# Kernel tuning notes

Hardware: AMD Instinct MI355X
Metric: run time of the kernel (lower is better)

The kernel has to match this reference:

```python
import jax, jax.numpy as jnp
import numpy as np

N_NODES = 100000
N_EDGES = 1200000
D = 64  # in = hid = out = 64


def _seg_sum(vals, idx, n):
    return jax.ops.segment_sum(vals, idx, num_segments=n)


def _graph_conv(x, src, dst, W, b, n_nodes):
    # dgl.nn.GraphConv with norm='both', bias=True:
    #   h = (D_out^-1/2 applied to src feats) -> sum over edges -> D_in^-1/2 -> +b
    # Weight applied first (math-equivalent linear, in==out dims here).
    e = src.shape[0]
    ones = jnp.ones((e,), x.dtype)
    deg_out = jnp.clip(_seg_sum(ones, src, n_nodes), 1.0)  # zero-deg clamp, as in DGL
    deg_in = jnp.clip(_seg_sum(ones, dst, n_nodes), 1.0)
    h = (x @ W) * jax.lax.rsqrt(deg_out)[:, None]          # [N, D]
    agg = _seg_sum(h[src], dst, n_nodes)                   # gather-scatter over edges
    return agg * jax.lax.rsqrt(deg_in)[:, None] + b


def _rgcn(x, edges, params, n_nodes):
    # HeteroGraphConv(aggregate='sum'): sum per-relation GraphConv outputs.
    (s0, d0), (s1, d1) = edges
    h = (_graph_conv(x, s0, d0, params['W1_0'], params['b1_0'], n_nodes)
         + _graph_conv(x, s1, d1, params['W1_1'], params['b1_1'], n_nodes))
    h = jax.nn.relu(h)
    h = (_graph_conv(h, s0, d0, params['W2_0'], params['b2_0'], n_nodes)
         + _graph_conv(h, s1, d1, params['W2_1'], params['b2_1'], n_nodes))
    return h


def setup_inputs() -> dict:
    key = jax.random.key(0)
    ks = jax.random.split(key, 16)
    inp = {
        'x': jax.random.normal(ks[0], (N_NODES, D), dtype=jnp.float32),
        'rel0_src': jax.random.randint(ks[1], (N_EDGES,), 0, N_NODES, dtype=jnp.int32),
        'rel0_dst': jax.random.randint(ks[2], (N_EDGES,), 0, N_NODES, dtype=jnp.int32),
        'rel1_src': jax.random.randint(ks[3], (N_EDGES,), 0, N_NODES, dtype=jnp.int32),
        'rel1_dst': jax.random.randint(ks[4], (N_EDGES,), 0, N_NODES, dtype=jnp.int32),
        'neg_src': jax.random.randint(ks[5], (N_EDGES,), 0, N_NODES, dtype=jnp.int32),
        'neg_dst': jax.random.randint(ks[6], (N_EDGES,), 0, N_NODES, dtype=jnp.int32),
    }
    scale = 1.0 / np.sqrt(D)
    for i, name in enumerate(['W1_0', 'W1_1', 'W2_0', 'W2_1']):
        inp[name] = jax.random.normal(ks[7 + i], (D, D), dtype=jnp.float32) * scale
    for name in ['b1_0', 'b1_1', 'b2_0', 'b2_1']:
        inp[name] = jnp.zeros((D,), dtype=jnp.float32)
    return inp


def reference(x, rel0_src, rel0_dst, rel1_src, rel1_dst, neg_src, neg_dst,
              W1_0, W1_1, W2_0, W2_1, b1_0, b1_1, b2_0, b2_1):
    params = {'W1_0': W1_0, 'b1_0': b1_0, 'W1_1': W1_1, 'b1_1': b1_1,
              'W2_0': W2_0, 'b2_0': b2_0, 'W2_1': W2_1, 'b2_1': b2_1}
    edges = ((rel0_src, rel0_dst), (rel1_src, rel1_dst))
    h = _rgcn(x, edges, params, N_NODES)  # [N, D]
    # HeteroDotProductPredictor: u_dot_v on etype edges -> [E, 1]
    pos_score = jnp.sum(h[rel0_src] * h[rel0_dst], axis=-1, keepdims=True)
    neg_score = jnp.sum(h[neg_src] * h[neg_dst], axis=-1, keepdims=True)
    return pos_score, neg_score
```

## Files before the change

kernel.cpp:

```cpp
#include <hip/hip_runtime.h>
#include <hip/hip_fp16.h>

#define N_NODES 100000
#define N_EDGES 1200000
#define TOTAL_E (2 * N_EDGES)
#define D 64

#define BSH 7
#define NBUCK 782
#define NCHUNK 320
#define CHUNK 7500
#define HIST_L (NBUCK * NCHUNK)
#define HIST2 (2 * HIST_L)
#define SCAN_BS 256
#define SCAN_NB2 ((HIST2 + SCAN_BS - 1) / SCAN_BS)
#define ENT_CAP 4608
#define L2M_GRID ((N_NODES + 127) / 128)
#define NKEY 2048

typedef __attribute__((ext_vector_type(8))) short bf16x8;
typedef __attribute__((ext_vector_type(4))) float f32x4;

__device__ __forceinline__ unsigned short f32_bf16_rne(float f) {
    unsigned u = __float_as_uint(f);
    unsigned r = u + 0x7FFF + ((u >> 16) & 1);
    return (unsigned short)(r >> 16);
}
__device__ __forceinline__ float bf16_f32(unsigned short h) {
    return __uint_as_float(((unsigned)h) << 16);
}

__global__ __launch_bounds__(512) void countA_kernel(const int* __restrict__ s0,
                                                     const int* __restrict__ d0,
                                                     const int* __restrict__ s1,
                                                     const int* __restrict__ d1,
                                                     int* __restrict__ hist) {
    __shared__ int hD[NBUCK];
    __shared__ int hS[NBUCK];
    int t = threadIdx.x;
    for (int i = t; i < NBUCK; i += 512) { hD[i] = 0; hS[i] = 0; }
    __syncthreads();
    int base = blockIdx.x * CHUNK;
    for (int i = t; i < CHUNK; i += 512) {
        int e = base + i;
        int rel = (e >= N_EDGES);
        int src = rel ? s1[e - N_EDGES] : s0[e];
        int dst = rel ? d1[e - N_EDGES] : d0[e];
        atomicAdd(&hD[dst >> BSH], 1);
        atomicAdd(&hS[src >> BSH], 1);
    }
    __syncthreads();
    for (int i = t; i < NBUCK; i += 512) {
        hist[i * NCHUNK + blockIdx.x] = hD[i];
        hist[HIST_L + i * NCHUNK + blockIdx.x] = hS[i];
    }
}

__global__ void scan1_kernel(const int* __restrict__ in, int* __restrict__ out,
                             int* __restrict__ bsum) {
    __shared__ int s[SCAN_BS];
    int t = threadIdx.x;
    int i = blockIdx.x * SCAN_BS + t;
    int v = (i < HIST2) ? in[i] : 0;
    s[t] = v;
    __syncthreads();
    for (int off = 1; off < SCAN_BS; off <<= 1) {
        int add = (t >= off) ? s[t - off] : 0;
        __syncthreads();
        s[t] += add;
        __syncthreads();
    }
    if (i < HIST2) out[i] = s[t] - v;
    if (t == SCAN_BS - 1) bsum[blockIdx.x] = s[t];
}

__global__ void scan2_kernel(int* __restrict__ bsum) {
    __shared__ int s[1024];
    int t = threadIdx.x;
    int v0 = (2 * t < SCAN_NB2) ? bsum[2 * t] : 0;
    int v1 = (2 * t + 1 < SCAN_NB2) ? bsum[2 * t + 1] : 0;
    int sum = v0 + v1;
    s[t] = sum;
    __syncthreads();
    for (int off = 1; off < 1024; off <<= 1) {
        int add = (t >= off) ? s[t - off] : 0;
        __syncthreads();
        s[t] += add;
        __syncthreads();
    }
    int ex = s[t] - sum;
    if (2 * t < SCAN_NB2) bsum[2 * t] = ex;
    if (2 * t + 1 < SCAN_NB2) bsum[2 * t + 1] = ex + v0;
}

__global__ void scan3_kernel(int* __restrict__ out, const int* __restrict__ bsum) {
    int i = blockIdx.x * SCAN_BS + threadIdx.x;
    if (i < HIST2) out[i] += bsum[blockIdx.x];
    if (i == 0) out[HIST2] = 2 * TOTAL_E;
}

__global__ __launch_bounds__(512) void scatterA_kernel(const int* __restrict__ s0,
                                                       const int* __restrict__ d0,
                                                       const int* __restrict__ s1,
                                                       const int* __restrict__ d1,
                                                       const int* __restrict__ OFS,
                                                       unsigned* __restrict__ binned,
                                                       unsigned char* __restrict__ binnedS) {
    __shared__ unsigned ent[CHUNK];
    __shared__ unsigned short kent[CHUNK];
    __shared__ int cnt[NBUCK], pfx[NBUCK], cur[NBUCK];
    __shared__ int tsum[512];
    int t = threadIdx.x, wg = blockIdx.x;
    int base = wg * CHUNK;

    for (int b = t; b < NBUCK; b += 512) cnt[b] = 0;
    __syncthreads();
    for (int i = t; i < CHUNK; i += 512) {
        int e = base + i;
        int rel = (e >= N_EDGES);
        int dst = rel ? d1[e - N_EDGES] : d0[e];
        atomicAdd(&cnt[dst >> BSH], 1);
    }
    __syncthreads();
    {
        int b2 = t * 2;
        int k0 = (b2 < NBUCK) ? cnt[b2] : 0;
        int k1 = (b2 + 1 < NBUCK) ? cnt[b2 + 1] : 0;
        int sum = k0 + k1;
        tsum[t] = sum;
        __syncthreads();
        for (int off = 1; off < 512; off <<= 1) {
            int add = (t >= off) ? tsum[t - off] : 0;
            __syncthreads();
            tsum[t] += add;
            __syncthreads();
        }
        int ex = tsum[t] - sum;
        if (b2 < NBUCK) pfx[b2] = ex;
        if (b2 + 1 < NBUCK) pfx[b2 + 1] = ex + k0;
    }
    __syncthreads();
    for (int b = t; b < NBUCK; b += 512) {
        cur[b] = pfx[b];
        cnt[b] = OFS[b * NCHUNK + wg];
    }
    __syncthreads();
    for (int i = t; i < CHUNK; i += 512) {
        int e = base + i;
        int rel = (e >= N_EDGES);
        int src = rel ? s1[e - N_EDGES] : s0[e];
        int dst = rel ? d1[e - N_EDGES] : d0[e];
        int kb = dst >> BSH;
        unsigned u = (unsigned)src | ((unsigned)(dst & 127) << 17) | ((unsigned)rel << 24);
        int r = atomicAdd(&cur[kb], 1);
        ent[r] = u;
        kent[r] = (unsigned short)kb;
    }
    __syncthreads();
    for (int j = t; j < CHUNK; j += 512) {
        int kb = (int)kent[j];
        binned[cnt[kb] + (j - pfx[kb])] = ent[j];
    }
    __syncthreads();
    for (int b = t; b < NBUCK; b += 512) cnt[b] = 0;
    __syncthreads();
    for (int i = t; i < CHUNK; i += 512)
        atomicAdd(&cnt[(int)(ent[i] & 0x1FFFFu) >> BSH], 1);
    __syncthreads();
    {
        int b2 = t * 2;
        int k0 = (b2 < NBUCK) ? cnt[b2] : 0;
        int k1 = (b2 + 1 < NBUCK) ? cnt[b2 + 1] : 0;
        int sum = k0 + k1;
        tsum[t] = sum;
        __syncthreads();
        for (int off = 1; off < 512; off <<= 1) {
            int add = (t >= off) ? tsum[t - off] : 0;
            __syncthreads();
            tsum[t] += add;
            __syncthreads();
        }
        int ex = tsum[t] - sum;
        if (b2 < NBUCK) pfx[b2] = ex;
        if (b2 + 1 < NBUCK) pfx[b2 + 1] = ex + k0;
    }
    __syncthreads();
    for (int b = t; b < NBUCK; b += 512) {
        cur[b] = pfx[b];
        cnt[b] = OFS[HIST_L + b * NCHUNK + wg] - TOTAL_E;
    }
    __syncthreads();
    for (int i = t; i < CHUNK; i += 512) {
        int kS = (int)(ent[i] & 0x1FFFFu) >> BSH;
        int r = atomicAdd(&cur[kS], 1);
        kent[r] = (unsigned short)i;
    }
    __syncthreads();
    for (int j = t; j < CHUNK; j += 512) {
        unsigned u = ent[(int)kent[j]];
        int kS = (int)(u & 0x1FFFFu) >> BSH;
        binnedS[cnt[kS] + (j - pfx[kS])] =
            (unsigned char)((u & 127) | (((u >> 24) & 1) << 7));
    }
}

__global__ __launch_bounds__(512) void sortB_kernel(unsigned* __restrict__ binned,
                                                    const int* __restrict__ OFS,
                                                    int* __restrict__ ip0,
                                                    int* __restrict__ ip1,
                                                    unsigned short* __restrict__ c0a,
                                                    unsigned short* __restrict__ c1a) {
    __shared__ unsigned ent[ENT_CAP];
    __shared__ int cnt[NKEY], pfx[NKEY], cur[NKEY];
    __shared__ int tsum[512];
    int t = threadIdx.x;
    int b = blockIdx.x;
    int start = OFS[b * NCHUNK];
    int end = OFS[(b + 1) * NCHUNK];
    int n = end - start;

    for (int i = t; i < NKEY; i += 512) cnt[i] = 0;
    __syncthreads();
    for (int i = t; i < n; i += 512) {
        unsigned u = binned[start + i];
        if (i < ENT_CAP) ent[i] = u;
        int key = ((int)((u >> 17) & 255) << 3) | (int)((u & 0x1FFFFu) >> 14);
        atomicAdd(&cnt[key], 1);
    }
    __syncthreads();
    int b4 = t * 4;
    int k0 = cnt[b4], k1 = cnt[b4 + 1], k2 = cnt[b4 + 2], k3 = cnt[b4 + 3];
    int s1 = k0 + k1, s2 = s1 + k2, s3 = s2 + k3;
    tsum[t] = s3;
    __syncthreads();
    for (int off = 1; off < 512; off <<= 1) {
        int add = (t >= off) ? tsum[t - off] : 0;
        __syncthreads();
        tsum[t] += add;
        __syncthreads();
    }
    int ex = tsum[t] - s3;
    pfx[b4] = ex;
    pfx[b4 + 1] = ex + k0;
    pfx[b4 + 2] = ex + s1;
    pfx[b4 + 3] = ex + s2;
    cur[b4] = ex;
    cur[b4 + 1] = ex + k0;
    cur[b4 + 2] = ex + s1;
    cur[b4 + 3] = ex + s2;
    __syncthreads();
    for (int i = t; i < n; i += 512) {
        if (i < ENT_CAP) {
            unsigned u = ent[i];
            int key = ((int)((u >> 17) & 255) << 3) | (int)((u & 0x1FFFFu) >> 14);
            int p = atomicAdd(&cur[key], 1);
            binned[start + p] = u & 0x1FFFF;
        }
    }
    if (t < 128) {
        int node = b * 128 + t;
        if (node < N_NODES) {
            int kr0 = t << 3;
            int kr1 = (1 << 10) | (t << 3);
            int p0 = pfx[kr0];
            int e0 = pfx[kr0 + 8];
            int p1 = pfx[kr1];
            int e1 = (t == 127) ? n : pfx[kr1 + 8];
            ip0[node] = start + p0;
            ip1[node] = start + p1;
            c0a[node] = (unsigned short)(e0 - p0);
            c1a[node] = (unsigned short)(e1 - p1);
        }
    }
}

__global__ __launch_bounds__(512) void countO_kernel(const unsigned char* __restrict__ binnedS,
                                                     const int* __restrict__ OFS,
                                                     int* __restrict__ cntO0,
                                                     int* __restrict__ cntO1) {
    __shared__ int cnt[256];
    int t = threadIdx.x;
    int b = blockIdx.x;
    int start = OFS[HIST_L + b * NCHUNK] - TOTAL_E;
    int end = OFS[HIST_L + (b + 1) * NCHUNK] - TOTAL_E;
    if (t < 256) cnt[t] = 0;
    __syncthreads();
    for (int i = start + t; i < end; i += 512)
        atomicAdd(&cnt[(int)binnedS[i]], 1);
    __syncthreads();
    if (t < 128) {
        int node = b * 128 + t;
        if (node < N_NODES) {
            cntO0[node] = cnt[t];
            cntO1[node] = cnt[t | 128];
        }
    }
}

__global__ void wprep_kernel(const float* __restrict__ W0,
                             const float* __restrict__ W1,
                             short* __restrict__ Wf) {
    int t = blockIdx.x * blockDim.x + threadIdx.x;
    if (t >= 2 * 4096) return;
    int rel = t >> 12;
    int e = t & 4095;
    int k = e >> 6, col = e & 63;
    float wv = (rel ? W1 : W0)[e];
    unsigned short hi = f32_bf16_rne(wv);
    unsigned short lo = f32_bf16_rne(wv - bf16_f32(hi));
    int kstep = k >> 5, g = (k >> 3) & 3, j = k & 7;
    int base = ((((rel * 2 + 0) * 2 + kstep) * 4 + g) * 64 + col) * 8 + j;
    int baseL = ((((rel * 2 + 1) * 2 + kstep) * 4 + g) * 64 + col) * 8 + j;
    Wf[base] = (short)hi;
    Wf[baseL] = (short)lo;
}

__global__ __launch_bounds__(256) void lin2m_kernel(const float* __restrict__ x,
                                                    const short* __restrict__ Wf,
                                                    const int* __restrict__ cntO0,
                                                    const int* __restrict__ cntO1,
                                                    __half* __restrict__ y0,
                                                    __half* __restrict__ y1) {
    int t = threadIdx.x;
    int w = t >> 6, lane = t & 63;
    int lr = lane & 15, g = lane >> 4;
    int rowbase = blockIdx.x * 128 + w * 32;

    bf16x8 ah[2][2], al[2][2];
#pragma unroll
    for (int m = 0; m < 2; ++m) {
        int row = rowbase + m * 16 + lr;
        bool ok = row < N_NODES;
        const float* xp = x + (size_t)row * 64 + g * 8;
#pragma unroll
        for (int s = 0; s < 2; ++s) {
            float fv[8];
            if (ok) {
                float4 f0 = ((const float4*)(xp + s * 32))[0];
                float4 f1 = ((const float4*)(xp + s * 32))[1];
                fv[0] = f0.x; fv[1] = f0.y; fv[2] = f0.z; fv[3] = f0.w;
                fv[4] = f1.x; fv[5] = f1.y; fv[6] = f1.z; fv[7] = f1.w;
            } else {
#pragma unroll
                for (int j = 0; j < 8; ++j) fv[j] = 0.f;
            }
#pragma unroll
            for (int j = 0; j < 8; ++j) {
                unsigned short hi = f32_bf16_rne(fv[j]);
                unsigned short lo = f32_bf16_rne(fv[j] - bf16_f32(hi));
                ah[m][s][j] = (short)hi;
                al[m][s][j] = (short)lo;
            }
        }
    }

    float rsc[2][2][4];
#pragma unroll
    for (int m = 0; m < 2; ++m)
#pragma unroll
        for (int reg = 0; reg < 4; ++reg) {
            int row = rowbase + m * 16 + g * 4 + reg;
            bool ok = row < N_NODES;
            rsc[0][m][reg] = ok ? rsqrtf((float)max(cntO0[row], 1)) : 1.f;
            rsc[1][m][reg] = ok ? rsqrtf((float)max(cntO1[row], 1)) : 1.f;
        }

#pragma unroll
    for (int rel = 0; rel < 2; ++rel) {
        __half* yo = rel ? y1 : y0;
        const short* wr = Wf + rel * 8192 + g * 512;
#pragma unroll
        for (int n = 0; n < 4; ++n) {
            const short* wb = wr + (n * 16 + lr) * 8;
            bf16x8 wh0 = *(const bf16x8*)(wb);
            bf16x8 wh1 = *(const bf16x8*)(wb + 2048);
            bf16x8 wl0 = *(const bf16x8*)(wb + 4096);
            bf16x8 wl1 = *(const bf16x8*)(wb + 6144);
#pragma unroll
            for (int m = 0; m < 2; ++m) {
                f32x4 acc = {0.f, 0.f, 0.f, 0.f};
                acc = __builtin_amdgcn_mfma_f32_16x16x32_bf16(al[m][0], wh0, acc, 0, 0, 0);
                acc = __builtin_amdgcn_mfma_f32_16x16x32_bf16(ah[m][0], wl0, acc, 0, 0, 0);
                acc = __builtin_amdgcn_mfma_f32_16x16x32_bf16(ah[m][0], wh0, acc, 0, 0, 0);
                acc = __builtin_amdgcn_mfma_f32_16x16x32_bf16(al[m][1], wh1, acc, 0, 0, 0);
                acc = __builtin_amdgcn_mfma_f32_16x16x32_bf16(ah[m][1], wl1, acc, 0, 0, 0);
                acc = __builtin_amdgcn_mfma_f32_16x16x32_bf16(ah[m][1], wh1, acc, 0, 0, 0);
#pragma unroll
                for (int reg = 0; reg < 4; ++reg) {
                    int row = rowbase + m * 16 + g * 4 + reg;
                    if (row < N_NODES)
                        yo[(size_t)row * 64 + n * 16 + lr] =
                            __float2half_rn(acc[reg] * rsc[rel][m][reg]);
                }
            }
        }
    }
}

template <int RELU, int OUTH>
__global__ __launch_bounds__(256) void aggC_kernel(const __half* __restrict__ L0,
                                                   const __half* __restrict__ L1,
                                                   const unsigned* __restrict__ es,
                                                   const int* __restrict__ ip0,
                                                   const int* __restrict__ ip1,
                                                   const unsigned short* __restrict__ c0a,
                                                   const unsigned short* __restrict__ c1a,
                                                   const float* __restrict__ bia0,
                                                   const float* __restrict__ bia1,
                                                   float* __restrict__ outf,
                                                   __half* __restrict__ outh) {
    int t = threadIdx.x;
    int g = t >> 3, l8 = t & 7;
    int node = blockIdx.x * 32 + g;
    if (node >= N_NODES) return;

    int st0 = ip0[node], c0 = c0a[node];
    int st1 = ip1[node], c1 = c1a[node];

    float a[8] = {0, 0, 0, 0, 0, 0, 0, 0};
    float a2[8] = {0, 0, 0, 0, 0, 0, 0, 0};
    float b[8] = {0, 0, 0, 0, 0, 0, 0, 0};
    float b2[8] = {0, 0, 0, 0, 0, 0, 0, 0};
    union HU { uint4 u; __half2 h[4]; };

    int k = 0;
    for (; k + 4 <= c0; k += 4) {
        int sA = (int)es[st0 + k];
        int sB = (int)es[st0 + k + 1];
        int sC = (int)es[st0 + k + 2];
        int sD = (int)es[st0 + k + 3];
        HU uA, uB, uC, uD;
        uA.u = ((const uint4*)(L0 + (size_t)sA * 64))[l8];
        uB.u = ((const uint4*)(L0 + (size_t)sB * 64))[l8];
        uC.u = ((const uint4*)(L0 + (size_t)sC * 64))[l8];
        uD.u = ((const uint4*)(L0 + (size_t)sD * 64))[l8];
#pragma unroll
        for (int q = 0; q < 4; ++q) {
            float2 fA = __half22float2(uA.h[q]);
            float2 fB = __half22float2(uB.h[q]);
            float2 fC = __half22float2(uC.h[q]);
            float2 fD = __half22float2(uD.h[q]);
            a[2 * q] += fA.x + fC.x;  a[2 * q + 1] += fA.y + fC.y;
            a2[2 * q] += fB.x + fD.x; a2[2 * q + 1] += fB.y + fD.y;
        }
    }
    for (; k < c0; ++k) {
        int s = (int)es[st0 + k];
        HU uu;
        uu.u = ((const uint4*)(L0 + (size_t)s * 64))[l8];
#pragma unroll
        for (int q = 0; q < 4; ++q) {
            float2 f = __half22float2(uu.h[q]);
            a[2 * q] += f.x;
            a[2 * q + 1] += f.y;
        }
    }
    k = 0;
    for (; k + 4 <= c1; k += 4) {
        int sA = (int)es[st1 + k];
        int sB = (int)es[st1 + k + 1];
        int sC = (int)es[st1 + k + 2];
        int sD = (int)es[st1 + k + 3];
        HU uA, uB, uC, uD;
        uA.u = ((const uint4*)(L1 + (size_t)sA * 64))[l8];
        uB.u = ((const uint4*)(L1 + (size_t)sB * 64))[l8];
        uC.u = ((const uint4*)(L1 + (size_t)sC * 64))[l8];
        uD.u = ((const uint4*)(L1 + (size_t)sD * 64))[l8];
#pragma unroll
        for (int q = 0; q < 4; ++q) {
            float2 fA = __half22float2(uA.h[q]);
            float2 fB = __half22float2(uB.h[q]);
            float2 fC = __half22float2(uC.h[q]);
            float2 fD = __half22float2(uD.h[q]);
            b[2 * q] += fA.x + fC.x;  b[2 * q + 1] += fA.y + fC.y;
            b2[2 * q] += fB.x + fD.x; b2[2 * q + 1] += fB.y + fD.y;
        }
    }
    for (; k < c1; ++k) {
        int s = (int)es[st1 + k];
        HU uu;
        uu.u = ((const uint4*)(L1 + (size_t)s * 64))[l8];
#pragma unroll
        for (int q = 0; q < 4; ++q) {
            float2 f = __half22float2(uu.h[q]);
            b[2 * q] += f.x;
            b[2 * q + 1] += f.y;
        }
    }

    float r0 = rsqrtf((float)max(c0, 1));
    float r1 = rsqrtf((float)max(c1, 1));
    float4 u0a = ((const float4*)bia0)[l8 * 2];
    float4 u0b = ((const float4*)bia0)[l8 * 2 + 1];
    float4 u1a = ((const float4*)bia1)[l8 * 2];
    float4 u1b = ((const float4*)bia1)[l8 * 2 + 1];
    float o[8];
#pragma unroll
    for (int q = 0; q < 8; ++q) o[q] = (a[q] + a2[q]) * r0 + (b[q] + b2[q]) * r1;
    o[0] += u0a.x + u1a.x; o[1] += u0a.y + u1a.y;
    o[2] += u0a.z + u1a.z; o[3] += u0a.w + u1a.w;
    o[4] += u0b.x + u1b.x; o[5] += u0b.y + u1b.y;
    o[6] += u0b.z + u1b.z; o[7] += u0b.w + u1b.w;
    if (RELU) {
#pragma unroll
        for (int q = 0; q < 8; ++q) o[q] = fmaxf(o[q], 0.f);
    }
    if (OUTH) {
        HU vv;
#pragma unroll
        for (int q = 0; q < 4; ++q)
            vv.h[q] = __floats2half2_rn(o[2 * q], o[2 * q + 1]);
        ((uint4*)(outh + (size_t)node * 64))[l8] = vv.u;
    } else {
        float4 f0 = {o[0], o[1], o[2], o[3]};
        float4 f1 = {o[4], o[5], o[6], o[7]};
        ((float4*)(outf + (size_t)node * 64))[l8 * 2] = f0;
        ((float4*)(outf + (size_t)node * 64))[l8 * 2 + 1] = f1;
    }
}

__global__ __launch_bounds__(256) void score_kernel(const __half* __restrict__ h2,
                                                    const int* __restrict__ ps,
                                                    const int* __restrict__ pd,
                                                    const int* __restrict__ ns,
                                                    const int* __restrict__ nd,
                                                    float* __restrict__ out) {
    int gid = blockIdx.x * blockDim.x + threadIdx.x;
    int pr = gid >> 3;
    int l8 = gid & 7;
    int e0 = pr * 2;
    if (e0 >= TOTAL_E) return;
    int e1 = e0 + 1;
    int sA, dA, sB, dB;
    if (e0 < N_EDGES) { sA = ps[e0]; dA = pd[e0]; sB = ps[e1]; dB = pd[e1]; }
    else {
        sA = ns[e0 - N_EDGES]; dA = nd[e0 - N_EDGES];
        sB = ns[e1 - N_EDGES]; dB = nd[e1 - N_EDGES];
    }
    union HU { uint4 u; __half2 h[4]; };
    HU ua0, ub0, ua1, ub1;
    ua0.u = ((const uint4*)(h2 + (size_t)sA * 64))[l8];
    ub0.u = ((const uint4*)(h2 + (size_t)dA * 64))[l8];
    ua1.u = ((const uint4*)(h2 + (size_t)sB * 64))[l8];
    ub1.u = ((const uint4*)(h2 + (size_t)dB * 64))[l8];
    float p0 = 0.f, p1 = 0.f;
#pragma unroll
    for (int q = 0; q < 4; ++q) {
        float2 fa0 = __half22float2(ua0.h[q]);
        float2 fb0 = __half22float2(ub0.h[q]);
        float2 fa1 = __half22float2(ua1.h[q]);
        float2 fb1 = __half22float2(ub1.h[q]);
        p0 += fa0.x * fb0.x + fa0.y * fb0.y;
        p1 += fa1.x * fb1.x + fa1.y * fb1.y;
    }
    p0 += __shfl_xor(p0, 1);
    p0 += __shfl_xor(p0, 2);
    p0 += __shfl_xor(p0, 4);
    p1 += __shfl_xor(p1, 1);
    p1 += __shfl_xor(p1, 2);
    p1 += __shfl_xor(p1, 4);
    if (l8 == 0) ((float2*)out)[pr] = make_float2(p0, p1);
}

extern "C" void kernel_launch(void* const* d_in, const int* in_sizes, int n_in,
                              void* d_out, int out_size, void* d_ws, size_t ws_size,
                              hipStream_t stream) {
    const float* x    = (const float*)d_in[0];
    const int* s0     = (const int*)d_in[1];
    const int* d0     = (const int*)d_in[2];
    const int* s1     = (const int*)d_in[3];
    const int* d1     = (const int*)d_in[4];
    const int* nsrc   = (const int*)d_in[5];
    const int* ndst   = (const int*)d_in[6];
    const float* W1_0 = (const float*)d_in[7];
    const float* W1_1 = (const float*)d_in[8];
    const float* W2_0 = (const float*)d_in[9];
    const float* W2_1 = (const float*)d_in[10];
    const float* b1_0 = (const float*)d_in[11];
    const float* b1_1 = (const float*)d_in[12];
    const float* b2_0 = (const float*)d_in[13];
    const float* b2_1 = (const float*)d_in[14];
    float* out = (float*)d_out;

    char* p = (char*)d_ws;
    int* cntO0 = (int*)p;      p += N_NODES * 4;
    int* cntO1 = (int*)p;      p += N_NODES * 4;
    int* hist  = (int*)p;      p += (size_t)HIST2 * 4;
    int* OFS   = (int*)p;      p += ((size_t)HIST2 + 8) * 4;
    int* bsum  = (int*)p;      p += 2048 * 4;
    unsigned* binned = (unsigned*)p;  p += (size_t)TOTAL_E * 4;
    int* ip0   = (int*)p;      p += N_NODES * 4;
    int* ip1   = (int*)p;      p += N_NODES * 4;
    unsigned short* c0a = (unsigned short*)p;  p += N_NODES * 2;
    unsigned short* c1a = (unsigned short*)p;  p += N_NODES * 2;
    unsigned char* binnedS = (unsigned char*)p;  p += (size_t)TOTAL_E;
    p = (char*)(((size_t)p + 255) & ~(size_t)255);
    short* WfA = (short*)p;    p += 16384 * 2;
    short* WfB = (short*)p;    p += 16384 * 2;
    p = (char*)(((size_t)p + 255) & ~(size_t)255);
    __half* bufL0h = (__half*)p;  p += (size_t)N_NODES * D * 2;
    __half* bufL1h = (__half*)p;  p += (size_t)N_NODES * D * 2;
    __half* h2h    = (__half*)p;  p += (size_t)N_NODES * D * 2;
    p = (char*)(((size_t)p + 255) & ~(size_t)255);
    float* bufH = (float*)p;   p += (size_t)N_NODES * D * 4;

    const int aggGrid  = (N_NODES + 31) / 32;
    const int scorGrid = (TOTAL_E / 2 * 8 + 255) / 256;

    wprep_kernel<<<32, 256, 0, stream>>>(W1_0, W1_1, WfA);
    wprep_kernel<<<32, 256, 0, stream>>>(W2_0, W2_1, WfB);

    countA_kernel<<<NCHUNK, 512, 0, stream>>>(s0, d0, s1, d1, hist);
    scan1_kernel<<<SCAN_NB2, SCAN_BS, 0, stream>>>(hist, OFS, bsum);
    scan2_kernel<<<1, 1024, 0, stream>>>(bsum);
    scan3_kernel<<<SCAN_NB2, SCAN_BS, 0, stream>>>(OFS, bsum);
    scatterA_kernel<<<NCHUNK, 512, 0, stream>>>(s0, d0, s1, d1, OFS, binned, binnedS);
    sortB_kernel<<<NBUCK, 512, 0, stream>>>(binned, OFS, ip0, ip1, c0a, c1a);
    countO_kernel<<<NBUCK, 512, 0, stream>>>(binnedS, OFS, cntO0, cntO1);

    lin2m_kernel<<<L2M_GRID, 256, 0, stream>>>(x, WfA, cntO0, cntO1, bufL0h, bufL1h);
    aggC_kernel<1, 0><<<aggGrid, 256, 0, stream>>>(bufL0h, bufL1h, binned, ip0, ip1,
                                                   c0a, c1a, b1_0, b1_1, bufH, nullptr);

    lin2m_kernel<<<L2M_GRID, 256, 0, stream>>>(bufH, WfB, cntO0, cntO1, bufL0h, bufL1h);
    aggC_kernel<0, 1><<<aggGrid, 256, 0, stream>>>(bufL0h, bufL1h, binned, ip0, ip1,
                                                   c0a, c1a, b2_0, b2_1, nullptr, h2h);

    score_kernel<<<scorGrid, 256, 0, stream>>>(h2h, s0, d0, nsrc, ndst, out);
}
```

Measured before the change: 273.3 us.

## Merge relation edge lists per node and gather in source-range phases

The edge sort now buckets each destination's incoming edges from both relations together, ordered by a coarse source-node range (13 phases), with the relation flag kept in bit 17. It records per-node phase counts. The aggregation kernel walks phases in lockstep across the block's 128 destination nodes, so concurrent gathers hit a narrower slice of the feature tables and should get better L2/cache locality. Per-edge degree scaling replaces the separate per-relation accumulators. The cost is a 16-entry count array per node, many more inner-loop iterations with small trip counts, and less unrolling (2 instead of 4), which may lower memory-level parallelism.

```diff
diff --git a/kernel.cpp b/kernel.cpp
--- a/kernel.cpp
+++ b/kernel.cpp
@@ -17,6 +17,7 @@
 #define ENT_CAP 4608
 #define L2M_GRID ((N_NODES + 127) / 128)
 #define NKEY 2048
+#define NPH 13
 
 typedef __attribute__((ext_vector_type(8))) short bf16x8;
 typedef __attribute__((ext_vector_type(4))) float f32x4;
@@ -206,12 +207,13 @@
 
 __global__ __launch_bounds__(512) void sortB_kernel(unsigned* __restrict__ binned,
                                                     const int* __restrict__ OFS,
-                                                    int* __restrict__ ip0,
-                                                    int* __restrict__ ip1,
+                                                    int* __restrict__ ip,
+                                                    unsigned short* __restrict__ cph,
                                                     unsigned short* __restrict__ c0a,
                                                     unsigned short* __restrict__ c1a) {
     __shared__ unsigned ent[ENT_CAP];
     __shared__ int cnt[NKEY], pfx[NKEY], cur[NKEY];
+    __shared__ int cnt2[256];
     __shared__ int tsum[512];
     int t = threadIdx.x;
     int b = blockIdx.x;
@@ -220,12 +222,15 @@
     int n = end - start;
 
     for (int i = t; i < NKEY; i += 512) cnt[i] = 0;
+    if (t < 256) cnt2[t] = 0;
     __syncthreads();
     for (int i = t; i < n; i += 512) {
         unsigned u = binned[start + i];
         if (i < ENT_CAP) ent[i] = u;
-        int key = ((int)((u >> 17) & 255) << 3) | (int)((u & 0x1FFFFu) >> 14);
-        atomicAdd(&cnt[key], 1);
+        int dl = (int)((u >> 17) & 127);
+        int ph = (int)((u & 0x1FFFFu) >> 13);
+        atomicAdd(&cnt[(dl << 4) | ph], 1);
+        atomicAdd(&cnt2[dl | (int)(((u >> 24) & 1) << 7)], 1);
     }
     __syncthreads();
     int b4 = t * 4;
@@ -252,24 +257,25 @@
     for (int i = t; i < n; i += 512) {
         if (i < ENT_CAP) {
             unsigned u = ent[i];
-            int key = ((int)((u >> 17) & 255) << 3) | (int)((u & 0x1FFFFu) >> 14);
-            int p = atomicAdd(&cur[key], 1);
-            binned[start + p] = u & 0x1FFFF;
+            int dl = (int)((u >> 17) & 127);
+            int ph = (int)((u & 0x1FFFFu) >> 13);
+            int p = atomicAdd(&cur[(dl << 4) | ph], 1);
+            binned[start + p] = (u & 0x1FFFFu) | (((u >> 24) & 1u) << 17);
         }
     }
     if (t < 128) {
         int node = b * 128 + t;
         if (node < N_NODES) {
-            int kr0 = t << 3;
-            int kr1 = (1 << 10) | (t << 3);
-            int p0 = pfx[kr0];
-            int e0 = pfx[kr0 + 8];
-            int p1 = pfx[kr1];
-            int e1 = (t == 127) ? n : pfx[kr1 + 8];
-            ip0[node] = start + p0;
-            ip1[node] = start + p1;
-            c0a[node] = (unsigned short)(e0 - p0);
-            c1a[node] = (unsigned short)(e1 - p1);
+            ip[node] = start + pfx[t << 4];
+            c0a[node] = (unsigned short)cnt2[t];
+            c1a[node] = (unsigned short)cnt2[t | 128];
+            unsigned short* cp = cph + (size_t)node * 16;
+#pragma unroll
+            for (int p2 = 0; p2 < 16; ++p2) {
+                int k = (t << 4) + p2;
+                int e2 = (k + 1 < NKEY) ? pfx[k + 1] : n;
+                cp[p2] = (unsigned short)((p2 < NPH) ? (e2 - pfx[k]) : 0);
+            }
         }
     }
 }
@@ -398,125 +404,114 @@
 }
 
 template <int RELU, int OUTH>
-__global__ __launch_bounds__(256) void aggC_kernel(const __half* __restrict__ L0,
+__global__ __launch_bounds__(512) void aggP_kernel(const __half* __restrict__ L0,
                                                    const __half* __restrict__ L1,
                                                    const unsigned* __restrict__ es,
-                                                   const int* __restrict__ ip0,
-                                                   const int* __restrict__ ip1,
+                                                   const int* __restrict__ ip,
+                                                   const unsigned short* __restrict__ cph,
                                                    const unsigned short* __restrict__ c0a,
                                                    const unsigned short* __restrict__ c1a,
                                                    const float* __restrict__ bia0,
                                                    const float* __restrict__ bia1,
                                                    float* __restrict__ outf,
                                                    __half* __restrict__ outh) {
-    int t = threadIdx.x;
+    int t = threadIdx.x, b = blockIdx.x;
     int g = t >> 3, l8 = t & 7;
-    int node = blockIdx.x * 32 + g;
-    if (node >= N_NODES) return;
-
-    int st0 = ip0[node], c0 = c0a[node];
-    int st1 = ip1[node], c1 = c1a[node];
-
-    float a[8] = {0, 0, 0, 0, 0, 0, 0, 0};
-    float a2[8] = {0, 0, 0, 0, 0, 0, 0, 0};
-    float b[8] = {0, 0, 0, 0, 0, 0, 0, 0};
-    float b2[8] = {0, 0, 0, 0, 0, 0, 0, 0};
+    int nA = b * 128 + g, nB = nA + 64;
+    bool vA = nA < N_NODES, vB = nB < N_NODES;
+    int curA = vA ? ip[nA] : 0;
+    int curB = vB ? ip[nB] : 0;
+    float rA0 = vA ? rsqrtf((float)max((int)c0a[nA], 1)) : 0.f;
+    float rA1 = vA ? rsqrtf((float)max((int)c1a[nA], 1)) : 0.f;
+    float rB0 = vB ? rsqrtf((float)max((int)c0a[nB], 1)) : 0.f;
+    float rB1 = vB ? rsqrtf((float)max((int)c1a[nB], 1)) : 0.f;
+    const unsigned short* cpA = cph + (size_t)nA * 16;
+    const unsigned short* cpB = cph + (size_t)nB * 16;
+
+    float oA[8] = {0, 0, 0, 0, 0, 0, 0, 0};
+    float oB[8] = {0, 0, 0, 0, 0, 0, 0, 0};
     union HU { uint4 u; __half2 h[4]; };
 
-    int k = 0;
-    for (; k + 4 <= c0; k += 4) {
-        int sA = (int)es[st0 + k];
-        int sB = (int)es[st0 + k + 1];
-        int sC = (int)es[st0 + k + 2];
-        int sD = (int)es[st0 + k + 3];
-        HU uA, uB, uC, uD;
-        uA.u = ((const uint4*)(L0 + (size_t)sA * 64))[l8];
-        uB.u = ((const uint4*)(L0 + (size_t)sB * 64))[l8];
-        uC.u = ((const uint4*)(L0 + (size_t)sC * 64))[l8];
-        uD.u = ((const uint4*)(L0 + (size_t)sD * 64))[l8];
-#pragma unroll
-        for (int q = 0; q < 4; ++q) {
-            float2 fA = __half22float2(uA.h[q]);
-            float2 fB = __half22float2(uB.h[q]);
-            float2 fC = __half22float2(uC.h[q]);
-            float2 fD = __half22float2(uD.h[q]);
-            a[2 * q] += fA.x + fC.x;  a[2 * q + 1] += fA.y + fC.y;
-            a2[2 * q] += fB.x + fD.x; a2[2 * q + 1] += fB.y + fD.y;
-        }
-    }
-    for (; k < c0; ++k) {
-        int s = (int)es[st0 + k];
-        HU uu;
-        uu.u = ((const uint4*)(L0 + (size_t)s * 64))[l8];
-#pragma unroll
-        for (int q = 0; q < 4; ++q) {
-            float2 f = __half22float2(uu.h[q]);
-            a[2 * q] += f.x;
-            a[2 * q + 1] += f.y;
-        }
-    }
-    k = 0;
-    for (; k + 4 <= c1; k += 4) {
-        int sA = (int)es[st1 + k];
-        int sB = (int)es[st1 + k + 1];
-        int sC = (int)es[st1 + k + 2];
-        int sD = (int)es[st1 + k + 3];
-        HU uA, uB, uC, uD;
-        uA.u = ((const uint4*)(L1 + (size_t)sA * 64))[l8];
-        uB.u = ((const uint4*)(L1 + (size_t)sB * 64))[l8];
-        uC.u = ((const uint4*)(L1 + (size_t)sC * 64))[l8];
-        uD.u = ((const uint4*)(L1 + (size_t)sD * 64))[l8];
-#pragma unroll
-        for (int q = 0; q < 4; ++q) {
-            float2 fA = __half22float2(uA.h[q]);
-            float2 fB = __half22float2(uB.h[q]);
-            float2 fC = __half22float2(uC.h[q]);
-            float2 fD = __half22float2(uD.h[q]);
-            b[2 * q] += fA.x + fC.x;  b[2 * q + 1] += fA.y + fC.y;
-            b2[2 * q] += fB.x + fD.x; b2[2 * q + 1] += fB.y + fD.y;
-        }
-    }
-    for (; k < c1; ++k) {
-        int s = (int)es[st1 + k];
-        HU uu;
-        uu.u = ((const uint4*)(L1 + (size_t)s * 64))[l8];
-#pragma unroll
-        for (int q = 0; q < 4; ++q) {
-            float2 f = __half22float2(uu.h[q]);
-            b[2 * q] += f.x;
-            b[2 * q + 1] += f.y;
-        }
-    }
-
-    float r0 = rsqrtf((float)max(c0, 1));
-    float r1 = rsqrtf((float)max(c1, 1));
+#define GATHER2(cur, c, o, r0_, r1_)                                          \
+    {                                                                         \
+        int k = 0;                                                            \
+        for (; k + 2 <= (c); k += 2) {                                        \
+            unsigned u1 = es[(cur) + k], u2 = es[(cur) + k + 1];              \
+            const __half* p1 = ((u1 >> 17) ? L1 : L0) + (size_t)(u1 & 0x1FFFFu) * 64; \
+            const __half* p2 = ((u2 >> 17) ? L1 : L0) + (size_t)(u2 & 0x1FFFFu) * 64; \
+            float sc1 = (u1 >> 17) ? (r1_) : (r0_);                           \
+            float sc2 = (u2 >> 17) ? (r1_) : (r0_);                           \
+            HU v1, v2;                                                        \
+            v1.u = ((const uint4*)p1)[l8];                                    \
+            v2.u = ((const uint4*)p2)[l8];                                    \
+            _Pragma("unroll")                                                 \
+            for (int q = 0; q < 4; ++q) {                                     \
+                float2 f1 = __half22float2(v1.h[q]);                          \
+                float2 f2 = __half22float2(v2.h[q]);                          \
+                (o)[2 * q] += f1.x * sc1 + f2.x * sc2;                        \
+                (o)[2 * q + 1] += f1.y * sc1 + f2.y * sc2;                    \
+            }                                                                 \
+        }                                                                     \
+        if (k < (c)) {                                                        \
+            unsigned u1 = es[(cur) + k];                                      \
+            const __half* p1 = ((u1 >> 17) ? L1 : L0) + (size_t)(u1 & 0x1FFFFu) * 64; \
+            float sc1 = (u1 >> 17) ? (r1_) : (r0_);                           \
+            HU v1;                                                            \
+            v1.u = ((const uint4*)p1)[l8];                                    \
+            _Pragma("unroll")                                                 \
+            for (int q = 0; q < 4; ++q) {                                     \
+                float2 f1 = __half22float2(v1.h[q]);                          \
+                (o)[2 * q] += f1.x * sc1;                                     \
+                (o)[2 * q + 1] += f1.y * sc1;                                 \
+            }                                                                 \
+        }                                                                     \
+    }
+
+    for (int p = 0; p < NPH; ++p) {
+        int cA = vA ? (int)cpA[p] : 0;
+        GATHER2(curA, cA, oA, rA0, rA1);
+        curA += cA;
+        int cB = vB ? (int)cpB[p] : 0;
+        GATHER2(curB, cB, oB, rB0, rB1);
+        curB += cB;
+    }
+#undef GATHER2
+
     float4 u0a = ((const float4*)bia0)[l8 * 2];
     float4 u0b = ((const float4*)bia0)[l8 * 2 + 1];
     float4 u1a = ((const float4*)bia1)[l8 * 2];
     float4 u1b = ((const float4*)bia1)[l8 * 2 + 1];
-    float o[8];
-#pragma unroll
-    for (int q = 0; q < 8; ++q) o[q] = (a[q] + a2[q]) * r0 + (b[q] + b2[q]) * r1;
-    o[0] += u0a.x + u1a.x; o[1] += u0a.y + u1a.y;
-    o[2] += u0a.z + u1a.z; o[3] += u0a.w + u1a.w;
-    o[4] += u0b.x + u1b.x; o[5] += u0b.y + u1b.y;
-    o[6] += u0b.z + u1b.z; o[7] += u0b.w + u1b.w;
-    if (RELU) {
-#pragma unroll
-        for (int q = 0; q < 8; ++q) o[q] = fmaxf(o[q], 0.f);
-    }
-    if (OUTH) {
-        HU vv;
-#pragma unroll
-        for (int q = 0; q < 4; ++q)
-            vv.h[q] = __floats2half2_rn(o[2 * q], o[2 * q + 1]);
-        ((uint4*)(outh + (size_t)node * 64))[l8] = vv.u;
-    } else {
-        float4 f0 = {o[0], o[1], o[2], o[3]};
-        float4 f1 = {o[4], o[5], o[6], o[7]};
-        ((float4*)(outf + (size_t)node * 64))[l8 * 2] = f0;
-        ((float4*)(outf + (size_t)node * 64))[l8 * 2 + 1] = f1;
-    }
+    float bs[8];
+    bs[0] = u0a.x + u1a.x; bs[1] = u0a.y + u1a.y;
+    bs[2] = u0a.z + u1a.z; bs[3] = u0a.w + u1a.w;
+    bs[4] = u0b.x + u1b.x; bs[5] = u0b.y + u1b.y;
+    bs[6] = u0b.z + u1b.z; bs[7] = u0b.w + u1b.w;
+
+#define STORE_NODE(valid, node, o)                                            \
+    if (valid) {                                                              \
+        float oo[8];                                                          \
+        _Pragma("unroll")                                                     \
+        for (int q = 0; q < 8; ++q) {                                         \
+            oo[q] = (o)[q] + bs[q];                                           \
+            if (RELU) oo[q] = fmaxf(oo[q], 0.f);                              \
+        }                                                                     \
+        if (OUTH) {                                                           \
+            HU vv;                                                            \
+            _Pragma("unroll")                                                 \
+            for (int q = 0; q < 4; ++q)                                       \
+                vv.h[q] = __floats2half2_rn(oo[2 * q], oo[2 * q + 1]);        \
+            ((uint4*)(outh + (size_t)(node) * 64))[l8] = vv.u;                \
+        } else {                                                              \
+            float4 f0 = {oo[0], oo[1], oo[2], oo[3]};                         \
+            float4 f1 = {oo[4], oo[5], oo[6], oo[7]};                         \
+            ((float4*)(outf + (size_t)(node) * 64))[l8 * 2] = f0;             \
+            ((float4*)(outf + (size_t)(node) * 64))[l8 * 2 + 1] = f1;         \
+        }                                                                     \
+    }
+
+    STORE_NODE(vA, nA, oA);
+    STORE_NODE(vB, nB, oB);
+#undef STORE_NODE
 }
 
 __global__ __launch_bounds__(256) void score_kernel(const __half* __restrict__ h2,
@@ -589,8 +584,8 @@
     int* OFS   = (int*)p;      p += ((size_t)HIST2 + 8) * 4;
     int* bsum  = (int*)p;      p += 2048 * 4;
     unsigned* binned = (unsigned*)p;  p += (size_t)TOTAL_E * 4;
-    int* ip0   = (int*)p;      p += N_NODES * 4;
-    int* ip1   = (int*)p;      p += N_NODES * 4;
+    int* ip    = (int*)p;      p += N_NODES * 4;
+    unsigned short* cph = (unsigned short*)p;  p += (size_t)(N_NODES) * 16 * 2;
     unsigned short* c0a = (unsigned short*)p;  p += N_NODES * 2;
     unsigned short* c1a = (unsigned short*)p;  p += N_NODES * 2;
     unsigned char* binnedS = (unsigned char*)p;  p += (size_t)TOTAL_E;
@@ -604,7 +599,6 @@
     p = (char*)(((size_t)p + 255) & ~(size_t)255);
     float* bufH = (float*)p;   p += (size_t)N_NODES * D * 4;
 
-    const int aggGrid  = (N_NODES + 31) / 32;
     const int scorGrid = (TOTAL_E / 2 * 8 + 255) / 256;
 
     wprep_kernel<<<32, 256, 0, stream>>>(W1_0, W1_1, WfA);
@@ -615,16 +609,16 @@
     scan2_kernel<<<1, 1024, 0, stream>>>(bsum);
     scan3_kernel<<<SCAN_NB2, SCAN_BS, 0, stream>>>(OFS, bsum);
     scatterA_kernel<<<NCHUNK, 512, 0, stream>>>(s0, d0, s1, d1, OFS, binned, binnedS);
-    sortB_kernel<<<NBUCK, 512, 0, stream>>>(binned, OFS, ip0, ip1, c0a, c1a);
+    sortB_kernel<<<NBUCK, 512, 0, stream>>>(binned, OFS, ip, cph, c0a, c1a);
     countO_kernel<<<NBUCK, 512, 0, stream>>>(binnedS, OFS, cntO0, cntO1);
 
     lin2m_kernel<<<L2M_GRID, 256, 0, stream>>>(x, WfA, cntO0, cntO1, bufL0h, bufL1h);
-    aggC_kernel<1, 0><<<aggGrid, 256, 0, stream>>>(bufL0h, bufL1h, binned, ip0, ip1,
-                                                   c0a, c1a, b1_0, b1_1, bufH, nullptr);
+    aggP_kernel<1, 0><<<NBUCK, 512, 0, stream>>>(bufL0h, bufL1h, binned, ip, cph,
+                                                 c0a, c1a, b1_0, b1_1, bufH, nullptr);
 
     lin2m_kernel<<<L2M_GRID, 256, 0, stream>>>(bufH, WfB, cntO0, cntO1, bufL0h, bufL1h);
-    aggC_kernel<0, 1><<<aggGrid, 256, 0, stream>>>(bufL0h, bufL1h, binned, ip0, ip1,
-                                                   c0a, c1a, b2_0, b2_1, nullptr, h2h);
+    aggP_kernel<0, 1><<<NBUCK, 512, 0, stream>>>(bufL0h, bufL1h, binned, ip, cph,
+                                                 c0a, c1a, b2_0, b2_1, nullptr, h2h);
 
     score_kernel<<<scorGrid, 256, 0, stream>>>(h2h, s0, d0, nsrc, ndst, out);
 }
```

New measurement: 421.8 us. 1.54x slower.

## Replace per-chunk histogram scan with global bucket totals and atomic offset claims

Applied to the files above, without the earlier changes.

Instead of writing a full per-chunk bucket histogram and running a three-kernel multi-block prefix scan, each chunk atomically accumulates global per-bucket totals, a single block scans the 782 buckets, and chunks claim their output ranges with atomicAdd on per-bucket cursors. The two weight-prep launches are also merged into one. This removes two kernel launches and the large histogram traffic. Chunk order within a bucket becomes nondeterministic, but sortB re-sorts each bucket so correctness should hold, though the per-edge order inside a node, and with it the floating-point summation order, may vary between runs.

```diff
diff --git a/kernel.cpp b/kernel.cpp
--- a/kernel.cpp
+++ b/kernel.cpp
@@ -10,10 +10,6 @@
 #define NBUCK 782
 #define NCHUNK 320
 #define CHUNK 7500
-#define HIST_L (NBUCK * NCHUNK)
-#define HIST2 (2 * HIST_L)
-#define SCAN_BS 256
-#define SCAN_NB2 ((HIST2 + SCAN_BS - 1) / SCAN_BS)
 #define ENT_CAP 4608
 #define L2M_GRID ((N_NODES + 127) / 128)
 #define NKEY 2048
@@ -34,7 +30,7 @@
                                                      const int* __restrict__ d0,
                                                      const int* __restrict__ s1,
                                                      const int* __restrict__ d1,
-                                                     int* __restrict__ hist) {
+                                                     int* __restrict__ tot) {
     __shared__ int hD[NBUCK];
     __shared__ int hS[NBUCK];
     int t = threadIdx.x;
@@ -51,36 +47,20 @@
     }
     __syncthreads();
     for (int i = t; i < NBUCK; i += 512) {
-        hist[i * NCHUNK + blockIdx.x] = hD[i];
-        hist[HIST_L + i * NCHUNK + blockIdx.x] = hS[i];
-    }
-}
-
-__global__ void scan1_kernel(const int* __restrict__ in, int* __restrict__ out,
-                             int* __restrict__ bsum) {
-    __shared__ int s[SCAN_BS];
-    int t = threadIdx.x;
-    int i = blockIdx.x * SCAN_BS + t;
-    int v = (i < HIST2) ? in[i] : 0;
-    s[t] = v;
-    __syncthreads();
-    for (int off = 1; off < SCAN_BS; off <<= 1) {
-        int add = (t >= off) ? s[t - off] : 0;
-        __syncthreads();
-        s[t] += add;
-        __syncthreads();
-    }
-    if (i < HIST2) out[i] = s[t] - v;
-    if (t == SCAN_BS - 1) bsum[blockIdx.x] = s[t];
-}
-
-__global__ void scan2_kernel(int* __restrict__ bsum) {
+        if (hD[i]) atomicAdd(&tot[i], hD[i]);
+        if (hS[i]) atomicAdd(&tot[NBUCK + i], hS[i]);
+    }
+}
+
+__global__ __launch_bounds__(1024) void scanB_kernel(const int* __restrict__ tot,
+                                                     int* __restrict__ dBase,
+                                                     int* __restrict__ sBase,
+                                                     int* __restrict__ curD,
+                                                     int* __restrict__ curS) {
     __shared__ int s[1024];
     int t = threadIdx.x;
-    int v0 = (2 * t < SCAN_NB2) ? bsum[2 * t] : 0;
-    int v1 = (2 * t + 1 < SCAN_NB2) ? bsum[2 * t + 1] : 0;
-    int sum = v0 + v1;
-    s[t] = sum;
+    int v = (t < NBUCK) ? tot[t] : 0;
+    s[t] = v;
     __syncthreads();
     for (int off = 1; off < 1024; off <<= 1) {
         int add = (t >= off) ? s[t - off] : 0;
@@ -88,22 +68,30 @@
         s[t] += add;
         __syncthreads();
     }
-    int ex = s[t] - sum;
-    if (2 * t < SCAN_NB2) bsum[2 * t] = ex;
-    if (2 * t + 1 < SCAN_NB2) bsum[2 * t + 1] = ex + v0;
-}
-
-__global__ void scan3_kernel(int* __restrict__ out, const int* __restrict__ bsum) {
-    int i = blockIdx.x * SCAN_BS + threadIdx.x;
-    if (i < HIST2) out[i] += bsum[blockIdx.x];
-    if (i == 0) out[HIST2] = 2 * TOTAL_E;
+    int ex = s[t] - v;
+    if (t < NBUCK) { dBase[t] = ex; curD[t] = ex; }
+    if (t == 0) dBase[NBUCK] = TOTAL_E;
+    __syncthreads();
+    int v2 = (t < NBUCK) ? tot[NBUCK + t] : 0;
+    s[t] = v2;
+    __syncthreads();
+    for (int off = 1; off < 1024; off <<= 1) {
+        int add = (t >= off) ? s[t - off] : 0;
+        __syncthreads();
+        s[t] += add;
+        __syncthreads();
+    }
+    int ex2 = s[t] - v2;
+    if (t < NBUCK) { sBase[t] = ex2; curS[t] = ex2; }
+    if (t == 0) sBase[NBUCK] = TOTAL_E;
 }
 
 __global__ __launch_bounds__(512) void scatterA_kernel(const int* __restrict__ s0,
                                                        const int* __restrict__ d0,
                                                        const int* __restrict__ s1,
                                                        const int* __restrict__ d1,
-                                                       const int* __restrict__ OFS,
+                                                       int* __restrict__ curD,
+                                                       int* __restrict__ curS,
                                                        unsigned* __restrict__ binned,
                                                        unsigned char* __restrict__ binnedS) {
     __shared__ unsigned ent[CHUNK];
@@ -142,7 +130,8 @@
     __syncthreads();
     for (int b = t; b < NBUCK; b += 512) {
         cur[b] = pfx[b];
-        cnt[b] = OFS[b * NCHUNK + wg];
+        int c = cnt[b];
+        cnt[b] = c ? atomicAdd(&curD[b], c) : 0;
     }
     __syncthreads();
     for (int i = t; i < CHUNK; i += 512) {
@@ -187,7 +176,8 @@
     __syncthreads();
     for (int b = t; b < NBUCK; b += 512) {
         cur[b] = pfx[b];
-        cnt[b] = OFS[HIST_L + b * NCHUNK + wg] - TOTAL_E;
+        int c = cnt[b];
+        cnt[b] = c ? atomicAdd(&curS[b], c) : 0;
     }
     __syncthreads();
     for (int i = t; i < CHUNK; i += 512) {
@@ -205,7 +195,7 @@
 }
 
 __global__ __launch_bounds__(512) void sortB_kernel(unsigned* __restrict__ binned,
-                                                    const int* __restrict__ OFS,
+                                                    const int* __restrict__ dBase,
                                                     int* __restrict__ ip0,
                                                     int* __restrict__ ip1,
                                                     unsigned short* __restrict__ c0a,
@@ -215,8 +205,8 @@
     __shared__ int tsum[512];
     int t = threadIdx.x;
     int b = blockIdx.x;
-    int start = OFS[b * NCHUNK];
-    int end = OFS[(b + 1) * NCHUNK];
+    int start = dBase[b];
+    int end = dBase[b + 1];
     int n = end - start;
 
     for (int i = t; i < NKEY; i += 512) cnt[i] = 0;
@@ -275,14 +265,14 @@
 }
 
 __global__ __launch_bounds__(512) void countO_kernel(const unsigned char* __restrict__ binnedS,
-                                                     const int* __restrict__ OFS,
+                                                     const int* __restrict__ sBase,
                                                      int* __restrict__ cntO0,
                                                      int* __restrict__ cntO1) {
     __shared__ int cnt[256];
     int t = threadIdx.x;
     int b = blockIdx.x;
-    int start = OFS[HIST_L + b * NCHUNK] - TOTAL_E;
-    int end = OFS[HIST_L + (b + 1) * NCHUNK] - TOTAL_E;
+    int start = sBase[b];
+    int end = sBase[b + 1];
     if (t < 256) cnt[t] = 0;
     __syncthreads();
     for (int i = start + t; i < end; i += 512)
@@ -297,15 +287,21 @@
     }
 }
 
-__global__ void wprep_kernel(const float* __restrict__ W0,
-                             const float* __restrict__ W1,
-                             short* __restrict__ Wf) {
+__global__ void wprep_kernel(const float* __restrict__ Wa0,
+                             const float* __restrict__ Wa1,
+                             const float* __restrict__ Wb0,
+                             const float* __restrict__ Wb1,
+                             short* __restrict__ WfA,
+                             short* __restrict__ WfB) {
     int t = blockIdx.x * blockDim.x + threadIdx.x;
-    if (t >= 2 * 4096) return;
-    int rel = t >> 12;
+    if (t >= 4 * 4096) return;
+    int layer = t >> 13;
+    int rel = (t >> 12) & 1;
     int e = t & 4095;
     int k = e >> 6, col = e & 63;
-    float wv = (rel ? W1 : W0)[e];
+    const float* W = layer ? (rel ? Wb1 : Wb0) : (rel ? Wa1 : Wa0);
+    short* Wf = layer ? WfB : WfA;
+    float wv = W[e];
     unsigned short hi = f32_bf16_rne(wv);
     unsigned short lo = f32_bf16_rne(wv - bf16_f32(hi));
     int kstep = k >> 5, g = (k >> 3) & 3, j = k & 7;
@@ -585,9 +581,11 @@
     char* p = (char*)d_ws;
     int* cntO0 = (int*)p;      p += N_NODES * 4;
     int* cntO1 = (int*)p;      p += N_NODES * 4;
-    int* hist  = (int*)p;      p += (size_t)HIST2 * 4;
-    int* OFS   = (int*)p;      p += ((size_t)HIST2 + 8) * 4;
-    int* bsum  = (int*)p;      p += 2048 * 4;
+    int* bucketTot = (int*)p;  p += 2 * NBUCK * 4;
+    int* dBase = (int*)p;      p += (NBUCK + 1) * 4;
+    int* sBase = (int*)p;      p += (NBUCK + 1) * 4;
+    int* curD  = (int*)p;      p += NBUCK * 4;
+    int* curS  = (int*)p;      p += NBUCK * 4;
     unsigned* binned = (unsigned*)p;  p += (size_t)TOTAL_E * 4;
     int* ip0   = (int*)p;      p += N_NODES * 4;
     int* ip1   = (int*)p;      p += N_NODES * 4;
@@ -607,16 +605,13 @@
     const int aggGrid  = (N_NODES + 31) / 32;
     const int scorGrid = (TOTAL_E / 2 * 8 + 255) / 256;
 
-    wprep_kernel<<<32, 256, 0, stream>>>(W1_0, W1_1, WfA);
-    wprep_kernel<<<32, 256, 0, stream>>>(W2_0, W2_1, WfB);
-
-    countA_kernel<<<NCHUNK, 512, 0, stream>>>(s0, d0, s1, d1, hist);
-    scan1_kernel<<<SCAN_NB2, SCAN_BS, 0, stream>>>(hist, OFS, bsum);
-    scan2_kernel<<<1, 1024, 0, stream>>>(bsum);
-    scan3_kernel<<<SCAN_NB2, SCAN_BS, 0, stream>>>(OFS, bsum);
-    scatterA_kernel<<<NCHUNK, 512, 0, stream>>>(s0, d0, s1, d1, OFS, binned, binnedS);
-    sortB_kernel<<<NBUCK, 512, 0, stream>>>(binned, OFS, ip0, ip1, c0a, c1a);
-    countO_kernel<<<NBUCK, 512, 0, stream>>>(binnedS, OFS, cntO0, cntO1);
+    hipMemsetAsync(bucketTot, 0, 2 * NBUCK * sizeof(int), stream);
+    wprep_kernel<<<64, 256, 0, stream>>>(W1_0, W1_1, W2_0, W2_1, WfA, WfB);
+    countA_kernel<<<NCHUNK, 512, 0, stream>>>(s0, d0, s1, d1, bucketTot);
+    scanB_kernel<<<1, 1024, 0, stream>>>(bucketTot, dBase, sBase, curD, curS);
+    scatterA_kernel<<<NCHUNK, 512, 0, stream>>>(s0, d0, s1, d1, curD, curS, binned, binnedS);
+    sortB_kernel<<<NBUCK, 512, 0, stream>>>(binned, dBase, ip0, ip1, c0a, c1a);
+    countO_kernel<<<NBUCK, 512, 0, stream>>>(binnedS, sBase, cntO0, cntO1);
 
     lin2m_kernel<<<L2M_GRID, 256, 0, stream>>>(x, WfA, cntO0, cntO1, bufL0h, bufL1h);
     aggC_kernel<1, 0><<<aggGrid, 256, 0, stream>>>(bufL0h, bufL1h, binned, ip0, ip1,
```

After: 281.3 us. 1.03x slower.
